# Kernel optimization log

Measured on AMD Instinct MI355X. Metric: run time of the kernel, lower is better.

## Reference

```python
import jax, jax.numpy as jnp
import numpy as np

N_LAYERS = 8
CODEBOOK_SIZE = 1024
DIM = 128


def setup_inputs() -> dict:
    key = jax.random.key(0)
    k1, k2 = jax.random.split(key)
    z = jax.random.normal(k1, (16, DIM, 4500), dtype=jnp.float32)
    # torch init: uniform(-1/K, 1/K); use small-scale values of similar magnitude
    codebooks = jax.random.uniform(
        k2, (N_LAYERS, CODEBOOK_SIZE, DIM), dtype=jnp.float32,
        minval=-1.0 / CODEBOOK_SIZE, maxval=1.0 / CODEBOOK_SIZE)
    return {"z": z, "codebooks": codebooks}


def reference(z, codebooks):
    """Residual VQ forward (update_mode='grad', eval mode: no EMA side effects).

    z: [B, D, T], codebooks: [L, K, D]
    Returns (quantized [B,D,T], all_layer_codes [L,B,T], loss_commit, loss_codebook).
    """
    B, D, T = z.shape
    zt = jnp.transpose(z, (0, 2, 1))  # [B, T, D]
    residual = zt
    z_q = jnp.zeros_like(zt)
    loss_commit = jnp.zeros((), dtype=zt.dtype)
    loss_codebook = jnp.zeros((), dtype=zt.dtype)
    all_codes = []
    for l in range(codebooks.shape[0]):  # sequential residual chain (small fixed L)
        cb = codebooks[l]  # [K, D]
        rf = residual.reshape(-1, D)  # [N, D]
        x2 = jnp.sum(rf * rf, axis=1, keepdims=True)
        y2 = jnp.sum(cb * cb, axis=1)[None, :]
        dist = x2 + y2 - 2.0 * (rf @ cb.T)
        idx = jnp.argmin(dist, axis=1)  # [N]
        q = cb[idx].reshape(B, T, D)
        qd = jax.lax.stop_gradient(q)
        loss_commit = loss_commit + jnp.mean((residual - qd) ** 2)
        loss_codebook = loss_codebook + jnp.mean((jax.lax.stop_gradient(residual) - q) ** 2)
        # straight-through estimator
        q_st = residual + jax.lax.stop_gradient(q - residual)
        z_q = z_q + q_st
        residual = residual - qd
        all_codes.append(idx.reshape(B, T))
    quantized = jnp.transpose(z_q, (0, 2, 1))  # [B, D, T]
    all_layer_codes = jnp.stack(all_codes, axis=0)  # [L, B, T]
    return quantized, all_layer_codes, loss_commit, loss_codebook
```

## Files before the change

kernel.cpp:

```cpp
#include <hip/hip_runtime.h>
#include <cstdint>
#include <cstddef>

#define B_ 16
#define D_ 128
#define T_ 4500
#define N_ (B_*T_)
#define K_ 1024
#define L_ 8
#define NRB 2250
#define NBLK 563
#define DELTA 4.0e-4f
#define BSCALE 16384.0f

typedef _Float16 f16x8 __attribute__((ext_vector_type(8)));
typedef float f32x16 __attribute__((ext_vector_type(16)));

#define GLOBAL_AS __attribute__((address_space(1)))
#define LDS_AS    __attribute__((address_space(3)))

__device__ __forceinline__ void ins3(float& p1, float& p2, float& p3, float x) {
  p3 = __builtin_amdgcn_fmed3f(p2, p3, x);
  p2 = __builtin_amdgcn_fmed3f(p1, p2, x);
  p1 = fminf(p1, x);
}
__device__ __forceinline__ void merge3(float& a1, float& a2, float& a3,
                                       float b1, float b2, float b3) {
  const float r3 = fminf(fminf(a3, b3), fminf(fmaxf(a2, b1), fmaxf(a1, b2)));
  const float r2 = fminf(fminf(fmaxf(a1, b1), a2), b2);
  const float r1 = fminf(a1, b1);
  a1 = r1; a2 = r2; a3 = r3;
}

__device__ __forceinline__ float pairwise_sq_sum128(const float* __restrict__ x) {
  float r[8];
#pragma unroll
  for (int c = 0; c < 8; ++c) r[c] = __fmul_rn(x[c], x[c]);
#pragma unroll
  for (int i = 1; i < 16; ++i)
#pragma unroll
    for (int c = 0; c < 8; ++c)
      r[c] = __fadd_rn(r[c], __fmul_rn(x[8*i + c], x[8*i + c]));
  return __fadd_rn(__fadd_rn(__fadd_rn(r[0], r[1]), __fadd_rn(r[2], r[3])),
                   __fadd_rn(__fadd_rn(r[4], r[5]), __fadd_rn(r[6], r[7])));
}

__device__ __forceinline__ float tree8(const float* rc) {
  return __fadd_rn(__fadd_rn(__fadd_rn(rc[0], rc[1]), __fadd_rn(rc[2], rc[3])),
                   __fadd_rn(__fadd_rn(rc[4], rc[5]), __fadd_rn(rc[6], rc[7])));
}

__global__ __launch_bounds__(256)
void k_transpose_z(const float* __restrict__ z, float* __restrict__ R) {
  __shared__ float tile[32][33];
  const int t0 = blockIdx.x * 32;
  const int d0 = blockIdx.y * 32;
  const int b  = blockIdx.z;
  const int tid = threadIdx.x;
  {
    const int jj = tid & 31; const int ii0 = (tid >> 5) * 4;
#pragma unroll
    for (int r = 0; r < 4; ++r) {
      const int ii = ii0 + r;
      float v = 0.f;
      if (t0 + jj < T_) v = z[((size_t)(b*D_ + d0 + ii))*T_ + t0 + jj];
      tile[ii][jj] = v;
    }
  }
  __syncthreads();
  {
    const int ii = tid & 31; const int jj0 = (tid >> 5) * 4;
#pragma unroll
    for (int r = 0; r < 4; ++r) {
      const int jj = jj0 + r;
      if (t0 + jj < T_)
        R[((size_t)(b*T_ + t0 + jj))*D_ + d0 + ii] = tile[ii][jj];
    }
  }
}

__global__ __launch_bounds__(256)
void k_transpose_cb(const float* __restrict__ cb, float* __restrict__ cbT) {
  __shared__ float tile[32][33];
  const int j0 = blockIdx.x * 32;
  const int d0 = blockIdx.y * 32;
  const int l  = blockIdx.z;
  const int tid = threadIdx.x;
  {
    const int dd = tid & 31; const int jj0 = (tid >> 5) * 4;
#pragma unroll
    for (int r = 0; r < 4; ++r)
      tile[jj0 + r][dd] = cb[((size_t)(l*K_ + j0 + jj0 + r))*D_ + d0 + dd];
  }
  __syncthreads();
  {
    const int jj = tid & 31; const int dd0 = (tid >> 5) * 4;
#pragma unroll
    for (int r = 0; r < 4; ++r)
      cbT[((size_t)(l*D_ + d0 + dd0 + r))*K_ + j0 + jj] = tile[jj][dd0 + r];
  }
}

__global__ __launch_bounds__(256)
void k_y2(const float* __restrict__ cb, float* __restrict__ y2f) {
  const int row = blockIdx.x * 256 + threadIdx.x;
  if (row >= L_ * K_) return;
  y2f[row] = pairwise_sq_sum128(&cb[(size_t)row * D_]);
}

__global__ __launch_bounds__(256)
void k_prep_b(const float* __restrict__ cb, uint4* __restrict__ Bpk) {
  const int tid = threadIdx.x;
  const int gw = blockIdx.x*4 + (tid >> 6);
  const int l = gw >> 5, cbk = gw & 31;
  const int lane = tid & 63, l31 = lane & 31, lh = lane >> 5;
  const int col = cbk*32 + l31;
  const float* src = cb + ((size_t)l*K_ + col)*D_ + lh*8;
  uint4* dst = Bpk + (size_t)l*16384 + (size_t)cbk*512;
#pragma unroll
  for (int s = 0; s < 8; ++s) {
    const float4 va = *(const float4*)(src + s*16);
    const float4 vb = *(const float4*)(src + s*16 + 4);
    f16x8 h;
    h[0] = (_Float16)(va.x * BSCALE); h[1] = (_Float16)(va.y * BSCALE);
    h[2] = (_Float16)(va.z * BSCALE); h[3] = (_Float16)(va.w * BSCALE);
    h[4] = (_Float16)(vb.x * BSCALE); h[5] = (_Float16)(vb.y * BSCALE);
    h[6] = (_Float16)(vb.z * BSCALE); h[7] = (_Float16)(vb.w * BSCALE);
    dst[s*64 + lane] = __builtin_bit_cast(uint4, h);
  }
}

__global__ __launch_bounds__(256)
void k_x2g(const float* __restrict__ R, float* __restrict__ x2) {
  const int tid = threadIdx.x;
  const int rowblk = blockIdx.x*4 + (tid >> 6);
  if (rowblk >= NRB) return;
  const int lane = tid & 63, l31 = lane & 31, lh = lane >> 5;
  const int row = rowblk*32 + l31;
  const float* rr = R + (size_t)row*D_ + lh*8;
  float rc[8] = {0,0,0,0,0,0,0,0};
#pragma unroll
  for (int s = 0; s < 8; ++s) {
    const float4 va = *(const float4*)(rr + s*16);
    const float4 vb = *(const float4*)(rr + s*16 + 4);
    const float rn[8] = {va.x, va.y, va.z, va.w, vb.x, vb.y, vb.z, vb.w};
#pragma unroll
    for (int c = 0; c < 8; ++c) {
      const float sq = __fmul_rn(rn[c], rn[c]);
      const float pv = __shfl_xor(sq, 32);
      rc[c] = __fadd_rn(rc[c], sq);
      rc[c] = __fadd_rn(rc[c], pv);
    }
  }
  if (lh == 0) x2[row] = tree8(rc);
}

__global__ __launch_bounds__(256, 3)
void k_layer(float* __restrict__ R, const uint4* __restrict__ Bpk_l,
             const float* __restrict__ y2l, const float* __restrict__ cbl,
             const float* __restrict__ cbTl, float* __restrict__ x2,
             float* __restrict__ out_codes, float* __restrict__ lossp)
{
  __shared__ uint4 Bs[2][1024];
  __shared__ float y2s[K_];
  __shared__ int2  rec[4][32];
  __shared__ float rs[4][128];
  const int tid = threadIdx.x;
  const int w = tid >> 6;
  const int lane = tid & 63, l31 = lane & 31, lh = lane >> 5;
  const int n0w = blockIdx.x*128 + w*32;
  const bool wactive = (n0w < N_);
  const int rbase = wactive ? n0w : 0;

#define STAGE(buf_, ch_) { \
    const uint4* sp_ = Bpk_l + (size_t)(ch_)*1024 + tid; \
    LDS_AS uint4* dp_ = (LDS_AS uint4*)&Bs[buf_][tid]; \
    _Pragma("unroll") \
    for (int i_ = 0; i_ < 4; ++i_) \
      __builtin_amdgcn_global_load_lds((const GLOBAL_AS void*)(sp_ + i_*256), \
                                       (LDS_AS void*)(dp_ + i_*256), 16, 0, 0); }

  STAGE(0, 0)

  {
    const float4 yv = *(const float4*)&y2l[tid*4];
    *(float4*)&y2s[tid*4] = yv;
  }

  f16x8 ah[8];
  {
    const float* rr = R + ((size_t)rbase + l31)*D_ + lh*8;
    float4 ra[8], rb[8];
#pragma unroll
    for (int s = 0; s < 8; ++s) {
      ra[s] = *(const float4*)(rr + s*16);
      rb[s] = *(const float4*)(rr + s*16 + 4);
    }
#pragma unroll
    for (int s = 0; s < 8; ++s) {
      f16x8 h;
      h[0] = (_Float16)ra[s].x; h[1] = (_Float16)ra[s].y;
      h[2] = (_Float16)ra[s].z; h[3] = (_Float16)ra[s].w;
      h[4] = (_Float16)rb[s].x; h[5] = (_Float16)rb[s].y;
      h[6] = (_Float16)rb[s].z; h[7] = (_Float16)rb[s].w;
      ah[s] = h;
    }
  }

  const float PINIT = __uint_as_float(0x7F7FFC00u);
  float p1[16], p2[16], p3[16];
#pragma unroll
  for (int r = 0; r < 16; ++r) { p1[r] = PINIT; p2[r] = PINIT; p3[r] = PINIT; }

  __syncthreads();

  for (int ch = 0; ch < 16; ++ch) {
    const int buf = ch & 1;
    if (ch < 15) {
      STAGE(buf ^ 1, ch + 1)
      asm volatile("s_waitcnt vmcnt(4)" ::: "memory");
    } else {
      asm volatile("s_waitcnt vmcnt(0)" ::: "memory");
    }
    __builtin_amdgcn_s_barrier();
    asm volatile("" ::: "memory");

    f32x16 acc0, acc1;
#pragma unroll
    for (int r = 0; r < 16; ++r) { acc0[r] = 0.f; acc1[r] = 0.f; }
    const uint4* bb = &Bs[buf][0];
    __builtin_amdgcn_s_setprio(1);
#pragma unroll
    for (int s = 0; s < 8; ++s) {
      const f16x8 b0 = __builtin_bit_cast(f16x8, bb[s*64 + lane]);
      const f16x8 b1 = __builtin_bit_cast(f16x8, bb[512 + s*64 + lane]);
      acc0 = __builtin_amdgcn_mfma_f32_32x32x16_f16(ah[s], b0, acc0, 0, 0, 0);
      acc1 = __builtin_amdgcn_mfma_f32_32x32x16_f16(ah[s], b1, acc1, 0, 0, 0);
    }
    __builtin_amdgcn_s_setprio(0);
    const float y2a = y2s[ch*64 + l31];
    const float y2b = y2s[ch*64 + 32 + l31];
    const unsigned ia = (unsigned)(ch*64 + l31);
    const unsigned ib = ia + 32;
#pragma unroll
    for (int r = 0; r < 16; ++r) {
      const float d0 = fmaf(-0x1p-13f, acc0[r], y2a);
      const float d1 = fmaf(-0x1p-13f, acc1[r], y2b);
      const float x0 = __uint_as_float((__float_as_uint(d0) & ~1023u) | ia);
      const float x1 = __uint_as_float((__float_as_uint(d1) & ~1023u) | ib);
      ins3(p1[r], p2[r], p3[r], x0);
      ins3(p1[r], p2[r], p3[r], x1);
    }
    asm volatile("" ::: "memory");
    __builtin_amdgcn_s_barrier();
  }
#undef STAGE

#pragma unroll
  for (int r = 0; r < 16; ++r) {
#pragma unroll
    for (int off = 1; off < 32; off <<= 1) {
      const float b1 = __shfl_xor(p1[r], off);
      const float b2 = __shfl_xor(p2[r], off);
      const float b3 = __shfl_xor(p3[r], off);
      merge3(p1[r], p2[r], p3[r], b1, b2, b3);
    }
    if (l31 == 0) {
      const int ri = (r&3) + 8*(r>>2) + 4*lh;
      int flags = 0;
      if (p3[r] - p1[r] <= DELTA) flags = 2;
      else if (p2[r] - p1[r] <= DELTA) flags = 1;
      rec[w][ri] = make_int2((int)(__float_as_uint(p1[r]) & 1023u) | (flags << 12),
                             (int)(__float_as_uint(p2[r]) & 1023u));
    }
  }
  asm volatile("s_waitcnt lgkmcnt(0)" ::: "memory");

  {
    bool doA = false; int cA1 = 0, cA2 = 0;
    if (wactive && lane < 32) {
      const int2 mr = rec[w][lane];
      if ((mr.x >> 12) == 1) { doA = true; cA1 = mr.x & 1023; cA2 = mr.y; }
    }
    if (doA) {
      const int n = rbase + lane;
      const float* xr = &R[(size_t)n*D_];
      const float* pa = &cbl[(size_t)cA1*D_];
      const float* pb = &cbl[(size_t)cA2*D_];
      float s1 = 0.f, s2 = 0.f;
#pragma unroll
      for (int k = 0; k < D_; k += 4) {
        const float4 x = *(const float4*)(xr + k);
        const float4 A = *(const float4*)(pa + k);
        const float4 Bv = *(const float4*)(pb + k);
        s1 = fmaf(x.x, A.x, s1);  s1 = fmaf(x.y, A.y, s1);
        s1 = fmaf(x.z, A.z, s1);  s1 = fmaf(x.w, A.w, s1);
        s2 = fmaf(x.x, Bv.x, s2); s2 = fmaf(x.y, Bv.y, s2);
        s2 = fmaf(x.z, Bv.z, s2); s2 = fmaf(x.w, Bv.w, s2);
      }
      const float x2n = x2[n];
      const float d1 = __fsub_rn(__fadd_rn(x2n, y2l[cA1]), __fmul_rn(2.f, s1));
      const float d2 = __fsub_rn(__fadd_rn(x2n, y2l[cA2]), __fmul_rn(2.f, s2));
      const bool take2 = (d2 < d1) || (d2 == d1 && cA2 < cA1);
      rec[w][lane] = make_int2(take2 ? cA2 : cA1, 0);
    }
    asm volatile("s_waitcnt lgkmcnt(0)" ::: "memory");
  }

  if (wactive) {
    for (int ri = 0; ri < 32; ++ri) {
      const int2 rr2 = rec[w][ri];
      if ((rr2.x >> 12) != 2) continue;
      const int n = rbase + ri;
      const float2 t = *(const float2*)&R[(size_t)n*D_ + lane*2];
      rs[w][lane*2] = t.x; rs[w][lane*2+1] = t.y;
      asm volatile("s_waitcnt lgkmcnt(0)" ::: "memory");
      const float x2n = x2[n];
      float acc[16];
#pragma unroll
      for (int q = 0; q < 16; ++q) acc[q] = 0.f;
      for (int k = 0; k < 128; ++k) {
        const float rv = rs[w][k];
        const float* cr = cbTl + (size_t)k*K_ + lane;
#pragma unroll
        for (int q = 0; q < 16; ++q)
          acc[q] = fmaf(rv, cr[q*64], acc[q]);
      }
      float vb = 3.0e38f; int jb = 0;
#pragma unroll
      for (int q = 0; q < 16; ++q) {
        const int j = q*64 + lane;
        const float dv = fmaf(-2.f, acc[q], __fadd_rn(x2n, y2l[j]));
        if (dv < vb) { vb = dv; jb = j; }
      }
#pragma unroll
      for (int off = 1; off < 64; off <<= 1) {
        const float bv = __shfl_xor(vb, off);
        const int   bj = __shfl_xor(jb, off);
        if (bv < vb || (bv == vb && bj < jb)) { vb = bv; jb = bj; }
      }
      if (lane == 0) rec[w][ri] = make_int2(jb, 0);
      asm volatile("s_waitcnt lgkmcnt(0)" ::: "memory");
    }
  }

  float ss = 0.f;
  if (wactive) {
    const int row = rbase + l31;
    const int code = rec[w][l31].x & 1023;
    float* rr = R + (size_t)row*D_ + lh*8;
    const float* cr = cbl + (size_t)code*D_ + lh*8;
    float4 xa[8], xb[8], qa[8], qb[8];
#pragma unroll
    for (int s = 0; s < 8; ++s) {
      xa[s] = *(const float4*)(rr + s*16);
      xb[s] = *(const float4*)(rr + s*16 + 4);
      qa[s] = *(const float4*)(cr + s*16);
      qb[s] = *(const float4*)(cr + s*16 + 4);
    }
    float rc[8] = {0,0,0,0,0,0,0,0};
#pragma unroll
    for (int s = 0; s < 8; ++s) {
      float rn[8];
      rn[0] = __fsub_rn(xa[s].x, qa[s].x); rn[1] = __fsub_rn(xa[s].y, qa[s].y);
      rn[2] = __fsub_rn(xa[s].z, qa[s].z); rn[3] = __fsub_rn(xa[s].w, qa[s].w);
      rn[4] = __fsub_rn(xb[s].x, qb[s].x); rn[5] = __fsub_rn(xb[s].y, qb[s].y);
      rn[6] = __fsub_rn(xb[s].z, qb[s].z); rn[7] = __fsub_rn(xb[s].w, qb[s].w);
      *(float4*)(rr + s*16)     = make_float4(rn[0], rn[1], rn[2], rn[3]);
      *(float4*)(rr + s*16 + 4) = make_float4(rn[4], rn[5], rn[6], rn[7]);
#pragma unroll
      for (int c = 0; c < 8; ++c) ss = fmaf(rn[c], rn[c], ss);
#pragma unroll
      for (int c = 0; c < 8; ++c) {
        const float sq = __fmul_rn(rn[c], rn[c]);
        const float pv = __shfl_xor(sq, 32);
        rc[c] = __fadd_rn(rc[c], sq);
        rc[c] = __fadd_rn(rc[c], pv);
      }
    }
    if (lh == 0) {
      x2[row] = tree8(rc);
      out_codes[row] = (float)code;
    }
  }
#pragma unroll
  for (int off = 1; off < 64; off <<= 1) ss += __shfl_xor(ss, off);
  if (wactive && lane == 0) atomicAdd(lossp, ss);
}

__global__ __launch_bounds__(256)
void k_finalize_quant(const float* __restrict__ z, const float* __restrict__ R,
                      float* __restrict__ out) {
  __shared__ float tile[32][33];
  const int t0 = blockIdx.x * 32;
  const int d0 = blockIdx.y * 32;
  const int b  = blockIdx.z;
  const int tid = threadIdx.x;
  {
    const int ii = tid & 31; const int jj0 = (tid >> 5) * 4;
#pragma unroll
    for (int r = 0; r < 4; ++r) {
      const int jj = jj0 + r;
      tile[ii][jj] = (t0 + jj < T_) ? R[((size_t)(b*T_ + t0 + jj))*D_ + d0 + ii] : 0.f;
    }
  }
  __syncthreads();
  {
    const int jj = tid & 31; const int ii0 = (tid >> 5) * 4;
#pragma unroll
    for (int r = 0; r < 4; ++r) {
      const int ii = ii0 + r;
      if (t0 + jj < T_) {
        const size_t gi = ((size_t)(b*D_ + d0 + ii))*T_ + t0 + jj;
        out[gi] = __fsub_rn(z[gi], tile[ii][jj]);
      }
    }
  }
}

__global__ void k_finalize_loss(const float* __restrict__ lossp, float* __restrict__ out2) {
  const float lv = (float)((double)lossp[0] / (double)((size_t)N_ * D_));
  out2[0] = lv;
  out2[1] = lv;
}

extern "C" void kernel_launch(void* const* d_in, const int* in_sizes, int n_in,
                              void* d_out, int out_size, void* d_ws, size_t ws_size,
                              hipStream_t stream) {
  const float* z  = (const float*)d_in[0];
  const float* cb = (const float*)d_in[1];
  float* out = (float*)d_out;

  char* ws = (char*)d_ws;
  const size_t OFF_R    = 0;
  const size_t OFF_BPK  = OFF_R   + (size_t)N_ * D_ * 4;
  const size_t OFF_CBT  = OFF_BPK + (size_t)L_ * 16384 * 16;
  const size_t OFF_Y2   = OFF_CBT + (size_t)L_ * D_ * K_ * 4;
  const size_t OFF_X2   = OFF_Y2  + (size_t)L_ * K_ * 4;
  const size_t OFF_LOSS = OFF_X2  + (size_t)N_ * 4;

  float* R     = (float*)(ws + OFF_R);
  uint4* Bpk   = (uint4*)(ws + OFF_BPK);
  float* cbT   = (float*)(ws + OFF_CBT);
  float* y2f   = (float*)(ws + OFF_Y2);
  float* x2    = (float*)(ws + OFF_X2);
  float* lossp = (float*)(ws + OFF_LOSS);

  hipMemsetAsync(lossp, 0, 4, stream);

  k_transpose_z<<<dim3((T_ + 31)/32, D_/32, B_), 256, 0, stream>>>(z, R);
  k_transpose_cb<<<dim3(K_/32, D_/32, L_), 256, 0, stream>>>(cb, cbT);
  k_y2<<<(L_ * K_)/256, 256, 0, stream>>>(cb, y2f);
  k_prep_b<<<64, 256, 0, stream>>>(cb, Bpk);
  k_x2g<<<563, 256, 0, stream>>>(R, x2);

  for (int l = 0; l < L_; ++l) {
    k_layer<<<NBLK, 256, 0, stream>>>(
        R,
        Bpk + (size_t)l * 16384,
        y2f + (size_t)l * K_,
        cb  + (size_t)l * K_ * D_,
        cbT + (size_t)l * D_ * K_,
        x2,
        out + (size_t)N_ * D_ + (size_t)l * N_,
        lossp);
  }

  k_finalize_quant<<<dim3((T_ + 31)/32, D_/32, B_), 256, 0, stream>>>(z, R, out);
  k_finalize_loss<<<1, 1, 0, stream>>>(lossp, out + (size_t)N_ * D_ + (size_t)L_ * N_);
}
```

Baseline: 949.9 us.

## Fuse all residual VQ layers into one persistent kernel with register-resident residuals

Replaces the separate x2 kernel and the eight per-layer launches with one kernel that loops over layers. Each block keeps its 128 residual rows in registers and their squared norms in shared memory, so R and x2 no longer go through global memory between layers. R is written back once at the end. The extra register pressure lowers the occupancy hint from 3 to 2 blocks per CU, and the refinement step now uses shuffles instead of reloading rows.

```diff
diff --git a/kernel.cpp b/kernel.cpp
--- a/kernel.cpp
+++ b/kernel.cpp
@@ -8,7 +8,6 @@
 #define N_ (B_*T_)
 #define K_ 1024
 #define L_ 8
-#define NRB 2250
 #define NBLK 563
 #define DELTA 4.0e-4f
 #define BSCALE 16384.0f
@@ -130,47 +129,62 @@
   }
 }
 
-__global__ __launch_bounds__(256)
-void k_x2g(const float* __restrict__ R, float* __restrict__ x2) {
-  const int tid = threadIdx.x;
-  const int rowblk = blockIdx.x*4 + (tid >> 6);
-  if (rowblk >= NRB) return;
-  const int lane = tid & 63, l31 = lane & 31, lh = lane >> 5;
-  const int row = rowblk*32 + l31;
-  const float* rr = R + (size_t)row*D_ + lh*8;
-  float rc[8] = {0,0,0,0,0,0,0,0};
-#pragma unroll
-  for (int s = 0; s < 8; ++s) {
-    const float4 va = *(const float4*)(rr + s*16);
-    const float4 vb = *(const float4*)(rr + s*16 + 4);
-    const float rn[8] = {va.x, va.y, va.z, va.w, vb.x, vb.y, vb.z, vb.w};
-#pragma unroll
-    for (int c = 0; c < 8; ++c) {
-      const float sq = __fmul_rn(rn[c], rn[c]);
-      const float pv = __shfl_xor(sq, 32);
-      rc[c] = __fadd_rn(rc[c], sq);
-      rc[c] = __fadd_rn(rc[c], pv);
-    }
-  }
-  if (lh == 0) x2[row] = tree8(rc);
-}
-
-__global__ __launch_bounds__(256, 3)
-void k_layer(float* __restrict__ R, const uint4* __restrict__ Bpk_l,
-             const float* __restrict__ y2l, const float* __restrict__ cbl,
-             const float* __restrict__ cbTl, float* __restrict__ x2,
-             float* __restrict__ out_codes, float* __restrict__ lossp)
+__global__ __launch_bounds__(256, 2)
+void k_rvq(float* __restrict__ R, const uint4* __restrict__ Bpk,
+           const float* __restrict__ y2f, const float* __restrict__ cb,
+           const float* __restrict__ cbT,
+           float* __restrict__ out_codes, float* __restrict__ lossp)
 {
   __shared__ uint4 Bs[2][1024];
   __shared__ float y2s[K_];
   __shared__ int2  rec[4][32];
   __shared__ float rs[4][128];
+  __shared__ float x2w[4][32];
   const int tid = threadIdx.x;
   const int w = tid >> 6;
   const int lane = tid & 63, l31 = lane & 31, lh = lane >> 5;
   const int n0w = blockIdx.x*128 + w*32;
   const bool wactive = (n0w < N_);
   const int rbase = wactive ? n0w : 0;
+  const int row = rbase + l31;
+  const bool hihalf = (lh != 0);
+
+  float4 xa[8], xb[8];
+  {
+    const float* rr = R + (size_t)row*D_ + lh*8;
+#pragma unroll
+    for (int s = 0; s < 8; ++s) {
+      xa[s] = *(const float4*)(rr + s*16);
+      xb[s] = *(const float4*)(rr + s*16 + 4);
+    }
+  }
+  {
+    float rc[8] = {0,0,0,0,0,0,0,0};
+#pragma unroll
+    for (int s = 0; s < 8; ++s) {
+      const float rn[8] = {xa[s].x, xa[s].y, xa[s].z, xa[s].w,
+                           xb[s].x, xb[s].y, xb[s].z, xb[s].w};
+#pragma unroll
+      for (int c = 0; c < 8; ++c) {
+        const float sq = __fmul_rn(rn[c], rn[c]);
+        const float pv = __shfl_xor(sq, 32);
+        rc[c] = __fadd_rn(rc[c], sq);
+        rc[c] = __fadd_rn(rc[c], pv);
+      }
+    }
+    if (lh == 0) x2w[w][l31] = tree8(rc);
+  }
+
+  float lsum = 0.f;
+  const float PINIT = __uint_as_float(0x7F7FFC00u);
+
+  for (int l = 0; l < L_; ++l) {
+    const uint4* Bpk_l = Bpk + (size_t)l*16384;
+    const float* y2l  = y2f + (size_t)l*K_;
+    const float* cbl  = cb  + (size_t)l*K_*D_;
+    const float* cbTl = cbT + (size_t)l*D_*K_;
+
+    __syncthreads();
 
 #define STAGE(buf_, ch_) { \
     const uint4* sp_ = Bpk_l + (size_t)(ch_)*1024 + tid; \
@@ -180,212 +194,229 @@
       __builtin_amdgcn_global_load_lds((const GLOBAL_AS void*)(sp_ + i_*256), \
                                        (LDS_AS void*)(dp_ + i_*256), 16, 0, 0); }
 
-  STAGE(0, 0)
-
-  {
-    const float4 yv = *(const float4*)&y2l[tid*4];
-    *(float4*)&y2s[tid*4] = yv;
-  }
-
-  f16x8 ah[8];
-  {
-    const float* rr = R + ((size_t)rbase + l31)*D_ + lh*8;
-    float4 ra[8], rb[8];
-#pragma unroll
-    for (int s = 0; s < 8; ++s) {
-      ra[s] = *(const float4*)(rr + s*16);
-      rb[s] = *(const float4*)(rr + s*16 + 4);
-    }
+    STAGE(0, 0)
+    {
+      const float4 yv = *(const float4*)&y2l[tid*4];
+      *(float4*)&y2s[tid*4] = yv;
+    }
+
+    f16x8 ah[8];
 #pragma unroll
     for (int s = 0; s < 8; ++s) {
       f16x8 h;
-      h[0] = (_Float16)ra[s].x; h[1] = (_Float16)ra[s].y;
-      h[2] = (_Float16)ra[s].z; h[3] = (_Float16)ra[s].w;
-      h[4] = (_Float16)rb[s].x; h[5] = (_Float16)rb[s].y;
-      h[6] = (_Float16)rb[s].z; h[7] = (_Float16)rb[s].w;
+      h[0] = (_Float16)xa[s].x; h[1] = (_Float16)xa[s].y;
+      h[2] = (_Float16)xa[s].z; h[3] = (_Float16)xa[s].w;
+      h[4] = (_Float16)xb[s].x; h[5] = (_Float16)xb[s].y;
+      h[6] = (_Float16)xb[s].z; h[7] = (_Float16)xb[s].w;
       ah[s] = h;
     }
-  }
-
-  const float PINIT = __uint_as_float(0x7F7FFC00u);
-  float p1[16], p2[16], p3[16];
-#pragma unroll
-  for (int r = 0; r < 16; ++r) { p1[r] = PINIT; p2[r] = PINIT; p3[r] = PINIT; }
-
-  __syncthreads();
-
-  for (int ch = 0; ch < 16; ++ch) {
-    const int buf = ch & 1;
-    if (ch < 15) {
-      STAGE(buf ^ 1, ch + 1)
-      asm volatile("s_waitcnt vmcnt(4)" ::: "memory");
-    } else {
-      asm volatile("s_waitcnt vmcnt(0)" ::: "memory");
-    }
-    __builtin_amdgcn_s_barrier();
-    asm volatile("" ::: "memory");
-
-    f32x16 acc0, acc1;
-#pragma unroll
-    for (int r = 0; r < 16; ++r) { acc0[r] = 0.f; acc1[r] = 0.f; }
-    const uint4* bb = &Bs[buf][0];
-    __builtin_amdgcn_s_setprio(1);
+
+    float p1[16], p2[16], p3[16];
+#pragma unroll
+    for (int r = 0; r < 16; ++r) { p1[r] = PINIT; p2[r] = PINIT; p3[r] = PINIT; }
+
+    __syncthreads();
+
+    for (int ch = 0; ch < 16; ++ch) {
+      const int buf = ch & 1;
+      if (ch < 15) {
+        STAGE(buf ^ 1, ch + 1)
+        asm volatile("s_waitcnt vmcnt(4)" ::: "memory");
+      } else {
+        asm volatile("s_waitcnt vmcnt(0)" ::: "memory");
+      }
+      __builtin_amdgcn_s_barrier();
+      asm volatile("" ::: "memory");
+
+      f32x16 acc0, acc1;
+#pragma unroll
+      for (int r = 0; r < 16; ++r) { acc0[r] = 0.f; acc1[r] = 0.f; }
+      const uint4* bb = &Bs[buf][0];
+      __builtin_amdgcn_s_setprio(1);
+#pragma unroll
+      for (int s = 0; s < 8; ++s) {
+        const f16x8 b0 = __builtin_bit_cast(f16x8, bb[s*64 + lane]);
+        const f16x8 b1 = __builtin_bit_cast(f16x8, bb[512 + s*64 + lane]);
+        acc0 = __builtin_amdgcn_mfma_f32_32x32x16_f16(ah[s], b0, acc0, 0, 0, 0);
+        acc1 = __builtin_amdgcn_mfma_f32_32x32x16_f16(ah[s], b1, acc1, 0, 0, 0);
+      }
+      __builtin_amdgcn_s_setprio(0);
+      const float y2a = y2s[ch*64 + l31];
+      const float y2b = y2s[ch*64 + 32 + l31];
+      const unsigned ia = (unsigned)(ch*64 + l31);
+      const unsigned ib = ia + 32;
+#pragma unroll
+      for (int r = 0; r < 16; ++r) {
+        const float d0 = fmaf(-0x1p-13f, acc0[r], y2a);
+        const float d1 = fmaf(-0x1p-13f, acc1[r], y2b);
+        const float x0 = __uint_as_float((__float_as_uint(d0) & ~1023u) | ia);
+        const float x1 = __uint_as_float((__float_as_uint(d1) & ~1023u) | ib);
+        ins3(p1[r], p2[r], p3[r], x0);
+        ins3(p1[r], p2[r], p3[r], x1);
+      }
+      asm volatile("" ::: "memory");
+      __builtin_amdgcn_s_barrier();
+    }
+#undef STAGE
+
+#pragma unroll
+    for (int r = 0; r < 16; ++r) {
+#pragma unroll
+      for (int off = 1; off < 32; off <<= 1) {
+        const float b1 = __shfl_xor(p1[r], off);
+        const float b2 = __shfl_xor(p2[r], off);
+        const float b3 = __shfl_xor(p3[r], off);
+        merge3(p1[r], p2[r], p3[r], b1, b2, b3);
+      }
+      if (l31 == 0) {
+        const int ri = (r&3) + 8*(r>>2) + 4*lh;
+        int flags = 0;
+        if (p3[r] - p1[r] <= DELTA) flags = 2;
+        else if (p2[r] - p1[r] <= DELTA) flags = 1;
+        rec[w][ri] = make_int2((int)(__float_as_uint(p1[r]) & 1023u) | (flags << 12),
+                               (int)(__float_as_uint(p2[r]) & 1023u));
+      }
+    }
+    asm volatile("s_waitcnt lgkmcnt(0)" ::: "memory");
+
+    {
+      const int2 mr = rec[w][l31];
+      const bool doA = wactive && ((mr.x >> 12) == 1);
+      const int cA1 = mr.x & 1023, cA2 = mr.y & 1023;
+      const float* pa = cbl + (size_t)cA1*D_;
+      const float* pb = cbl + (size_t)cA2*D_;
+      float s1 = 0.f, s2 = 0.f;
+#pragma unroll
+      for (int s = 0; s < 8; ++s) {
+        const float o0 = xa[s].x, o1 = xa[s].y, o2 = xa[s].z, o3 = xa[s].w;
+        const float o4 = xb[s].x, o5 = xb[s].y, o6 = xb[s].z, o7 = xb[s].w;
+        const float q0 = __shfl_xor(o0, 32), q1 = __shfl_xor(o1, 32);
+        const float q2 = __shfl_xor(o2, 32), q3 = __shfl_xor(o3, 32);
+        const float q4 = __shfl_xor(o4, 32), q5 = __shfl_xor(o5, 32);
+        const float q6 = __shfl_xor(o6, 32), q7 = __shfl_xor(o7, 32);
+        const float L0 = hihalf?q0:o0, L1 = hihalf?q1:o1, L2 = hihalf?q2:o2, L3 = hihalf?q3:o3;
+        const float L4 = hihalf?q4:o4, L5 = hihalf?q5:o5, L6 = hihalf?q6:o6, L7 = hihalf?q7:o7;
+        const float H0 = hihalf?o0:q0, H1 = hihalf?o1:q1, H2 = hihalf?o2:q2, H3 = hihalf?o3:q3;
+        const float H4 = hihalf?o4:q4, H5 = hihalf?o5:q5, H6 = hihalf?o6:q6, H7 = hihalf?o7:q7;
+        if (doA) {
+          const float4 A0 = *(const float4*)(pa + s*16);
+          const float4 A1 = *(const float4*)(pa + s*16 + 4);
+          const float4 A2 = *(const float4*)(pa + s*16 + 8);
+          const float4 A3 = *(const float4*)(pa + s*16 + 12);
+          const float4 B0 = *(const float4*)(pb + s*16);
+          const float4 B1 = *(const float4*)(pb + s*16 + 4);
+          const float4 B2 = *(const float4*)(pb + s*16 + 8);
+          const float4 B3 = *(const float4*)(pb + s*16 + 12);
+          s1 = fmaf(L0,A0.x,s1); s1 = fmaf(L1,A0.y,s1); s1 = fmaf(L2,A0.z,s1); s1 = fmaf(L3,A0.w,s1);
+          s1 = fmaf(L4,A1.x,s1); s1 = fmaf(L5,A1.y,s1); s1 = fmaf(L6,A1.z,s1); s1 = fmaf(L7,A1.w,s1);
+          s1 = fmaf(H0,A2.x,s1); s1 = fmaf(H1,A2.y,s1); s1 = fmaf(H2,A2.z,s1); s1 = fmaf(H3,A2.w,s1);
+          s1 = fmaf(H4,A3.x,s1); s1 = fmaf(H5,A3.y,s1); s1 = fmaf(H6,A3.z,s1); s1 = fmaf(H7,A3.w,s1);
+          s2 = fmaf(L0,B0.x,s2); s2 = fmaf(L1,B0.y,s2); s2 = fmaf(L2,B0.z,s2); s2 = fmaf(L3,B0.w,s2);
+          s2 = fmaf(L4,B1.x,s2); s2 = fmaf(L5,B1.y,s2); s2 = fmaf(L6,B1.z,s2); s2 = fmaf(L7,B1.w,s2);
+          s2 = fmaf(H0,B2.x,s2); s2 = fmaf(H1,B2.y,s2); s2 = fmaf(H2,B2.z,s2); s2 = fmaf(H3,B2.w,s2);
+          s2 = fmaf(H4,B3.x,s2); s2 = fmaf(H5,B3.y,s2); s2 = fmaf(H6,B3.z,s2); s2 = fmaf(H7,B3.w,s2);
+        }
+      }
+      if (doA) {
+        const float x2n = x2w[w][l31];
+        const float d1 = __fsub_rn(__fadd_rn(x2n, y2l[cA1]), __fmul_rn(2.f, s1));
+        const float d2 = __fsub_rn(__fadd_rn(x2n, y2l[cA2]), __fmul_rn(2.f, s2));
+        const bool take2 = (d2 < d1) || (d2 == d1 && cA2 < cA1);
+        if (lh == 0) rec[w][l31] = make_int2(take2 ? cA2 : cA1, 0);
+      }
+      asm volatile("s_waitcnt lgkmcnt(0)" ::: "memory");
+    }
+
+    if (wactive) {
+      for (int ri = 0; ri < 32; ++ri) {
+        const int2 rr2 = rec[w][ri];
+        if ((rr2.x >> 12) != 2) continue;
+        if (l31 == ri) {
+          float* dst = &rs[w][lh*8];
+#pragma unroll
+          for (int s = 0; s < 8; ++s) {
+            *(float4*)(dst + s*16)     = xa[s];
+            *(float4*)(dst + s*16 + 4) = xb[s];
+          }
+        }
+        asm volatile("s_waitcnt lgkmcnt(0)" ::: "memory");
+        const float x2n = x2w[w][ri];
+        float acc[16];
+#pragma unroll
+        for (int q = 0; q < 16; ++q) acc[q] = 0.f;
+        for (int k = 0; k < 128; ++k) {
+          const float rv = rs[w][k];
+          const float* cr = cbTl + (size_t)k*K_ + lane;
+#pragma unroll
+          for (int q = 0; q < 16; ++q)
+            acc[q] = fmaf(rv, cr[q*64], acc[q]);
+        }
+        float vb = 3.0e38f; int jb = 0;
+#pragma unroll
+        for (int q = 0; q < 16; ++q) {
+          const int j = q*64 + lane;
+          const float dv = fmaf(-2.f, acc[q], __fadd_rn(x2n, y2l[j]));
+          if (dv < vb) { vb = dv; jb = j; }
+        }
+#pragma unroll
+        for (int off = 1; off < 64; off <<= 1) {
+          const float bv = __shfl_xor(vb, off);
+          const int   bj = __shfl_xor(jb, off);
+          if (bv < vb || (bv == vb && bj < jb)) { vb = bv; jb = bj; }
+        }
+        if (lane == 0) rec[w][ri] = make_int2(jb, 0);
+        asm volatile("s_waitcnt lgkmcnt(0)" ::: "memory");
+      }
+    }
+
+    if (wactive) {
+      const int code = rec[w][l31].x & 1023;
+      const float* cr = cbl + (size_t)code*D_ + lh*8;
+      float4 qa[8], qb[8];
+#pragma unroll
+      for (int s = 0; s < 8; ++s) {
+        qa[s] = *(const float4*)(cr + s*16);
+        qb[s] = *(const float4*)(cr + s*16 + 4);
+      }
+      float rc[8] = {0,0,0,0,0,0,0,0};
+#pragma unroll
+      for (int s = 0; s < 8; ++s) {
+        float rn[8];
+        rn[0] = __fsub_rn(xa[s].x, qa[s].x); rn[1] = __fsub_rn(xa[s].y, qa[s].y);
+        rn[2] = __fsub_rn(xa[s].z, qa[s].z); rn[3] = __fsub_rn(xa[s].w, qa[s].w);
+        rn[4] = __fsub_rn(xb[s].x, qb[s].x); rn[5] = __fsub_rn(xb[s].y, qb[s].y);
+        rn[6] = __fsub_rn(xb[s].z, qb[s].z); rn[7] = __fsub_rn(xb[s].w, qb[s].w);
+        xa[s] = make_float4(rn[0], rn[1], rn[2], rn[3]);
+        xb[s] = make_float4(rn[4], rn[5], rn[6], rn[7]);
+#pragma unroll
+        for (int c = 0; c < 8; ++c) lsum = fmaf(rn[c], rn[c], lsum);
+#pragma unroll
+        for (int c = 0; c < 8; ++c) {
+          const float sq = __fmul_rn(rn[c], rn[c]);
+          const float pv = __shfl_xor(sq, 32);
+          rc[c] = __fadd_rn(rc[c], sq);
+          rc[c] = __fadd_rn(rc[c], pv);
+        }
+      }
+      if (lh == 0) {
+        x2w[w][l31] = tree8(rc);
+        out_codes[(size_t)l*N_ + row] = (float)code;
+      }
+    }
+    asm volatile("s_waitcnt lgkmcnt(0)" ::: "memory");
+  }
+
+  if (wactive) {
+    float* rr = R + (size_t)row*D_ + lh*8;
 #pragma unroll
     for (int s = 0; s < 8; ++s) {
-      const f16x8 b0 = __builtin_bit_cast(f16x8, bb[s*64 + lane]);
-      const f16x8 b1 = __builtin_bit_cast(f16x8, bb[512 + s*64 + lane]);
-      acc0 = __builtin_amdgcn_mfma_f32_32x32x16_f16(ah[s], b0, acc0, 0, 0, 0);
-      acc1 = __builtin_amdgcn_mfma_f32_32x32x16_f16(ah[s], b1, acc1, 0, 0, 0);
-    }
-    __builtin_amdgcn_s_setprio(0);
-    const float y2a = y2s[ch*64 + l31];
-    const float y2b = y2s[ch*64 + 32 + l31];
-    const unsigned ia = (unsigned)(ch*64 + l31);
-    const unsigned ib = ia + 32;
-#pragma unroll
-    for (int r = 0; r < 16; ++r) {
-      const float d0 = fmaf(-0x1p-13f, acc0[r], y2a);
-      const float d1 = fmaf(-0x1p-13f, acc1[r], y2b);
-      const float x0 = __uint_as_float((__float_as_uint(d0) & ~1023u) | ia);
-      const float x1 = __uint_as_float((__float_as_uint(d1) & ~1023u) | ib);
-      ins3(p1[r], p2[r], p3[r], x0);
-      ins3(p1[r], p2[r], p3[r], x1);
-    }
-    asm volatile("" ::: "memory");
-    __builtin_amdgcn_s_barrier();
-  }
-#undef STAGE
-
-#pragma unroll
-  for (int r = 0; r < 16; ++r) {
-#pragma unroll
-    for (int off = 1; off < 32; off <<= 1) {
-      const float b1 = __shfl_xor(p1[r], off);
-      const float b2 = __shfl_xor(p2[r], off);
-      const float b3 = __shfl_xor(p3[r], off);
-      merge3(p1[r], p2[r], p3[r], b1, b2, b3);
-    }
-    if (l31 == 0) {
-      const int ri = (r&3) + 8*(r>>2) + 4*lh;
-      int flags = 0;
-      if (p3[r] - p1[r] <= DELTA) flags = 2;
-      else if (p2[r] - p1[r] <= DELTA) flags = 1;
-      rec[w][ri] = make_int2((int)(__float_as_uint(p1[r]) & 1023u) | (flags << 12),
-                             (int)(__float_as_uint(p2[r]) & 1023u));
-    }
-  }
-  asm volatile("s_waitcnt lgkmcnt(0)" ::: "memory");
-
-  {
-    bool doA = false; int cA1 = 0, cA2 = 0;
-    if (wactive && lane < 32) {
-      const int2 mr = rec[w][lane];
-      if ((mr.x >> 12) == 1) { doA = true; cA1 = mr.x & 1023; cA2 = mr.y; }
-    }
-    if (doA) {
-      const int n = rbase + lane;
-      const float* xr = &R[(size_t)n*D_];
-      const float* pa = &cbl[(size_t)cA1*D_];
-      const float* pb = &cbl[(size_t)cA2*D_];
-      float s1 = 0.f, s2 = 0.f;
-#pragma unroll
-      for (int k = 0; k < D_; k += 4) {
-        const float4 x = *(const float4*)(xr + k);
-        const float4 A = *(const float4*)(pa + k);
-        const float4 Bv = *(const float4*)(pb + k);
-        s1 = fmaf(x.x, A.x, s1);  s1 = fmaf(x.y, A.y, s1);
-        s1 = fmaf(x.z, A.z, s1);  s1 = fmaf(x.w, A.w, s1);
-        s2 = fmaf(x.x, Bv.x, s2); s2 = fmaf(x.y, Bv.y, s2);
-        s2 = fmaf(x.z, Bv.z, s2); s2 = fmaf(x.w, Bv.w, s2);
-      }
-      const float x2n = x2[n];
-      const float d1 = __fsub_rn(__fadd_rn(x2n, y2l[cA1]), __fmul_rn(2.f, s1));
-      const float d2 = __fsub_rn(__fadd_rn(x2n, y2l[cA2]), __fmul_rn(2.f, s2));
-      const bool take2 = (d2 < d1) || (d2 == d1 && cA2 < cA1);
-      rec[w][lane] = make_int2(take2 ? cA2 : cA1, 0);
-    }
-    asm volatile("s_waitcnt lgkmcnt(0)" ::: "memory");
-  }
-
-  if (wactive) {
-    for (int ri = 0; ri < 32; ++ri) {
-      const int2 rr2 = rec[w][ri];
-      if ((rr2.x >> 12) != 2) continue;
-      const int n = rbase + ri;
-      const float2 t = *(const float2*)&R[(size_t)n*D_ + lane*2];
-      rs[w][lane*2] = t.x; rs[w][lane*2+1] = t.y;
-      asm volatile("s_waitcnt lgkmcnt(0)" ::: "memory");
-      const float x2n = x2[n];
-      float acc[16];
-#pragma unroll
-      for (int q = 0; q < 16; ++q) acc[q] = 0.f;
-      for (int k = 0; k < 128; ++k) {
-        const float rv = rs[w][k];
-        const float* cr = cbTl + (size_t)k*K_ + lane;
-#pragma unroll
-        for (int q = 0; q < 16; ++q)
-          acc[q] = fmaf(rv, cr[q*64], acc[q]);
-      }
-      float vb = 3.0e38f; int jb = 0;
-#pragma unroll
-      for (int q = 0; q < 16; ++q) {
-        const int j = q*64 + lane;
-        const float dv = fmaf(-2.f, acc[q], __fadd_rn(x2n, y2l[j]));
-        if (dv < vb) { vb = dv; jb = j; }
-      }
-#pragma unroll
-      for (int off = 1; off < 64; off <<= 1) {
-        const float bv = __shfl_xor(vb, off);
-        const int   bj = __shfl_xor(jb, off);
-        if (bv < vb || (bv == vb && bj < jb)) { vb = bv; jb = bj; }
-      }
-      if (lane == 0) rec[w][ri] = make_int2(jb, 0);
-      asm volatile("s_waitcnt lgkmcnt(0)" ::: "memory");
-    }
-  }
-
-  float ss = 0.f;
-  if (wactive) {
-    const int row = rbase + l31;
-    const int code = rec[w][l31].x & 1023;
-    float* rr = R + (size_t)row*D_ + lh*8;
-    const float* cr = cbl + (size_t)code*D_ + lh*8;
-    float4 xa[8], xb[8], qa[8], qb[8];
-#pragma unroll
-    for (int s = 0; s < 8; ++s) {
-      xa[s] = *(const float4*)(rr + s*16);
-      xb[s] = *(const float4*)(rr + s*16 + 4);
-      qa[s] = *(const float4*)(cr + s*16);
-      qb[s] = *(const float4*)(cr + s*16 + 4);
-    }
-    float rc[8] = {0,0,0,0,0,0,0,0};
-#pragma unroll
-    for (int s = 0; s < 8; ++s) {
-      float rn[8];
-      rn[0] = __fsub_rn(xa[s].x, qa[s].x); rn[1] = __fsub_rn(xa[s].y, qa[s].y);
-      rn[2] = __fsub_rn(xa[s].z, qa[s].z); rn[3] = __fsub_rn(xa[s].w, qa[s].w);
-      rn[4] = __fsub_rn(xb[s].x, qb[s].x); rn[5] = __fsub_rn(xb[s].y, qb[s].y);
-      rn[6] = __fsub_rn(xb[s].z, qb[s].z); rn[7] = __fsub_rn(xb[s].w, qb[s].w);
-      *(float4*)(rr + s*16)     = make_float4(rn[0], rn[1], rn[2], rn[3]);
-      *(float4*)(rr + s*16 + 4) = make_float4(rn[4], rn[5], rn[6], rn[7]);
-#pragma unroll
-      for (int c = 0; c < 8; ++c) ss = fmaf(rn[c], rn[c], ss);
-#pragma unroll
-      for (int c = 0; c < 8; ++c) {
-        const float sq = __fmul_rn(rn[c], rn[c]);
-        const float pv = __shfl_xor(sq, 32);
-        rc[c] = __fadd_rn(rc[c], sq);
-        rc[c] = __fadd_rn(rc[c], pv);
-      }
-    }
-    if (lh == 0) {
-      x2[row] = tree8(rc);
-      out_codes[row] = (float)code;
-    }
-  }
-#pragma unroll
-  for (int off = 1; off < 64; off <<= 1) ss += __shfl_xor(ss, off);
-  if (wactive && lane == 0) atomicAdd(lossp, ss);
+      *(float4*)(rr + s*16)     = xa[s];
+      *(float4*)(rr + s*16 + 4) = xb[s];
+    }
+  }
+#pragma unroll
+  for (int off = 1; off < 64; off <<= 1) lsum += __shfl_xor(lsum, off);
+  if (wactive && lane == 0) atomicAdd(lossp, lsum);
 }
 
 __global__ __launch_bounds__(256)
@@ -436,14 +467,12 @@
   const size_t OFF_BPK  = OFF_R   + (size_t)N_ * D_ * 4;
   const size_t OFF_CBT  = OFF_BPK + (size_t)L_ * 16384 * 16;
   const size_t OFF_Y2   = OFF_CBT + (size_t)L_ * D_ * K_ * 4;
-  const size_t OFF_X2   = OFF_Y2  + (size_t)L_ * K_ * 4;
-  const size_t OFF_LOSS = OFF_X2  + (size_t)N_ * 4;
+  const size_t OFF_LOSS = OFF_Y2  + (size_t)L_ * K_ * 4;
 
   float* R     = (float*)(ws + OFF_R);
   uint4* Bpk   = (uint4*)(ws + OFF_BPK);
   float* cbT   = (float*)(ws + OFF_CBT);
   float* y2f   = (float*)(ws + OFF_Y2);
-  float* x2    = (float*)(ws + OFF_X2);
   float* lossp = (float*)(ws + OFF_LOSS);
 
   hipMemsetAsync(lossp, 0, 4, stream);
@@ -452,19 +481,9 @@
   k_transpose_cb<<<dim3(K_/32, D_/32, L_), 256, 0, stream>>>(cb, cbT);
   k_y2<<<(L_ * K_)/256, 256, 0, stream>>>(cb, y2f);
   k_prep_b<<<64, 256, 0, stream>>>(cb, Bpk);
-  k_x2g<<<563, 256, 0, stream>>>(R, x2);
-
-  for (int l = 0; l < L_; ++l) {
-    k_layer<<<NBLK, 256, 0, stream>>>(
-        R,
-        Bpk + (size_t)l * 16384,
-        y2f + (size_t)l * K_,
-        cb  + (size_t)l * K_ * D_,
-        cbT + (size_t)l * D_ * K_,
-        x2,
-        out + (size_t)N_ * D_ + (size_t)l * N_,
-        lossp);
-  }
+
+  k_rvq<<<NBLK, 256, 0, stream>>>(R, Bpk, y2f, cb, cbT,
+                                  out + (size_t)N_ * D_, lossp);
 
   k_finalize_quant<<<dim3((T_ + 31)/32, D_/32, B_), 256, 0, stream>>>(z, R, out);
   k_finalize_loss<<<1, 1, 0, stream>>>(lossp, out + (size_t)N_ * D_ + (size_t)L_ * N_);
```

Measured after the change: 791.5 us. -16.7%, faster.
